# Kernel tuning notes

Hardware: AMD Instinct MI355X
Metric: run time of the kernel (lower is better)

The kernel has to match this reference:

```python
import jax, jax.numpy as jnp
import numpy as np

B, S, D = 8, 2048, 1024
N = 256          # state_dim
H = 512          # selector_hidden
E = 8            # num_experts


def murmurhash3_finalizer(token_ids):
    # Torch code works in int64 but masks to 32 bits after each multiply and
    # values stay non-negative, so it is exactly uint32 wrapping arithmetic.
    x = token_ids.astype(jnp.uint32)
    x = x ^ (x >> 16)
    x = x * jnp.uint32(2246822507)
    x = x ^ (x >> 13)
    x = x * jnp.uint32(3266489909)
    x = x ^ (x >> 16)
    return x


def setup_inputs() -> dict:
    key = jax.random.key(0)
    ks = jax.random.split(key, 7)
    scale = 0.02
    return {
        "x": jax.random.normal(ks[0], (B, S, D), dtype=jnp.float32),
        "token_ids": jax.random.randint(ks[1], (B, S), 0, 50257, dtype=jnp.int32),
        "Win": jax.random.normal(ks[2], (E, N, D), dtype=jnp.float32) * scale,      # in_proj.weight per expert
        "Wsin": jax.random.normal(ks[3], (E, H, D), dtype=jnp.float32) * scale,     # selector_in.weight
        "Wsout": jax.random.normal(ks[4], (E, 4 * N, H), dtype=jnp.float32) * scale,  # selector_out.weight
        "Wout": jax.random.normal(ks[5], (E, D, N), dtype=jnp.float32) * scale,     # out_proj.weight
        "dparam": jnp.ones((E, N), dtype=jnp.float32),                              # per-expert d
    }


def _forward(x, Win, Wsin, Wsout, Wout, dparam, token_ids):
    b, s, d = x.shape
    e_num, n, _ = Win.shape
    routes = (murmurhash3_finalizer(token_ids) % jnp.uint32(e_num)).astype(jnp.int32)  # (B,S)

    # Per-token expert projections, selected by hash route (masked accumulation
    # over the small fixed expert count; honors per-token routing).
    u = jnp.zeros((b, s, n), x.dtype)
    a = jnp.zeros((b, s, n), x.dtype)
    bg = jnp.zeros((b, s, n), x.dtype)
    c = jnp.zeros((b, s, n), x.dtype)
    dg = jnp.zeros((b, s, n), x.dtype)
    for e in range(e_num):
        m = (routes == e)[..., None]
        u = jnp.where(m, jnp.einsum('bsd,nd->bsn', x, Win[e]), u)
        sh = jax.nn.silu(jnp.einsum('bsd,hd->bsh', x, Wsin[e]))
        sel = jnp.einsum('bsh,oh->bso', sh, Wsout[e])       # (B,S,4N)
        ar, br, cr, dr = jnp.split(sel, 4, axis=-1)
        a = jnp.where(m, jax.nn.sigmoid(ar), a)
        bg = jnp.where(m, jnp.tanh(br), bg)
        c = jnp.where(m, jnp.tanh(cr), c)
        dg = jnp.where(m, jax.nn.sigmoid(dr), dg)

    dvec = dparam[routes]              # (B,S,N) expert d param per token
    skip = dvec * dg * u               # residual term, state-independent

    bidx = jnp.arange(b)

    def step(states, inp):
        # states: (B,E,N) per-expert hidden state per batch row
        route_t, u_t, a_t, b_t, c_t, skip_t = inp
        h_prev = states[bidx, route_t]                 # (B,N)
        h = a_t * h_prev + b_t * u_t
        states = states.at[bidx, route_t].set(h)       # only routed expert updates
        y = c_t * h + skip_t
        return states, y

    xs = (routes.swapaxes(0, 1), u.swapaxes(0, 1), a.swapaxes(0, 1),
          bg.swapaxes(0, 1), c.swapaxes(0, 1), skip.swapaxes(0, 1))
    states0 = jnp.zeros((b, e_num, n), x.dtype)
    _, ys = jax.lax.scan(step, states0, xs)            # ys: (S,B,N)
    y = ys.swapaxes(0, 1)                              # (B,S,N)

    out = jnp.zeros((b, s, d), x.dtype)
    for e in range(e_num):
        m = (routes == e)[..., None]
        out = jnp.where(m, jnp.einsum('bsn,dn->bsd', y, Wout[e]), out)
    return out


def reference(x, token_ids, Win, Wsin, Wsout, Wout, dparam):
    return _forward(x, Win, Wsin, Wsout, Wout, dparam, token_ids)
```

## Files before the change

### kernel.cpp

```cpp
#include <hip/hip_runtime.h>


#define TOKS 16384
#define RPAD 16512
#define DD   1024
#define NN   256
#define HH   512
#define MAXTILES  136
#define MAXCHUNKS 1088
#define CHUNK 16

typedef short short8 __attribute__((ext_vector_type(8)));
typedef float floatx4 __attribute__((ext_vector_type(4)));
typedef _Float16 half_t;

#define AS_GLOBAL __attribute__((address_space(1)))
#define AS_LDS    __attribute__((address_space(3)))

__device__ __forceinline__ void gl_lds16(const void* g, void* l) {
    __builtin_amdgcn_global_load_lds((const AS_GLOBAL void*)g, (AS_LDS void*)l, 16, 0, 0);
}

__device__ __forceinline__ unsigned short f2bf(float f) {
    union { float f; unsigned u; } c; c.f = f;
    unsigned r = c.u + 0x7FFF + ((c.u >> 16) & 1);
    return (unsigned short)(r >> 16);
}
__device__ __forceinline__ int route_of(int token) {
    unsigned x = (unsigned)token;
    x ^= x >> 16; x *= 2246822507u; x ^= x >> 13; x *= 3266489909u; x ^= x >> 16;
    return (int)(x & 7u);
}
__device__ __forceinline__ float sigm(float v) { return 1.0f / (1.0f + __expf(-v)); }
__device__ __forceinline__ float ftanh(float v) {
    float e = __expf(2.0f * v);
    return 1.0f - 2.0f / (e + 1.0f);
}

__global__ void k_route(const int* __restrict__ tok, int* __restrict__ cnt) {
    int b = blockIdx.x, tid = threadIdx.x;
    __shared__ int lc[256 * 8];
    #pragma unroll
    for (int e = 0; e < 8; e++) lc[tid * 8 + e] = 0;
    #pragma unroll
    for (int i = 0; i < 8; i++) {
        int e = route_of(tok[b * 2048 + tid * 8 + i]);
        lc[tid * 8 + e]++;
    }
    __syncthreads();
    if (tid < 8) {
        int s = 0;
        for (int t = 0; t < 256; t++) s += lc[t * 8 + tid];
        cnt[b * 8 + tid] = s;
    }
}

__global__ void k_offsets(const int* __restrict__ cnt, int* __restrict__ grpoff,
                          int* __restrict__ tileE, int* __restrict__ tileS,
                          int* __restrict__ tileR,
                          int* __restrict__ cGrp, int* __restrict__ cStart,
                          int* __restrict__ cLen, int* __restrict__ gBase,
                          int* __restrict__ meta) {
    __shared__ int sc[64], ce[8], eoff[9], etile[9], gb[65], go[64];
    int tid = threadIdx.x;
    if (tid < 64) sc[tid] = cnt[tid];
    __syncthreads();
    if (tid < 8) { int s = 0; for (int b = 0; b < 8; b++) s += sc[b * 8 + tid]; ce[tid] = s; }
    __syncthreads();
    if (tid == 0) {
        eoff[0] = 0; etile[0] = 0;
        for (int e = 0; e < 8; e++) {
            eoff[e + 1] = eoff[e] + ce[e];
            etile[e + 1] = etile[e] + (ce[e] + 127) / 128;
        }
        meta[0] = etile[8];
        gb[0] = 0;
        for (int g = 0; g < 64; g++) gb[g + 1] = gb[g] + (sc[g] + CHUNK - 1) / CHUNK;
        meta[1] = gb[64];
    }
    __syncthreads();
    if (tid < 64) {
        int b = tid >> 3, e = tid & 7;
        int run = eoff[e];
        for (int b2 = 0; b2 < b; b2++) run += sc[b2 * 8 + e];
        go[tid] = run;
        grpoff[tid] = run;
    }
    __syncthreads();
    if (tid < 8) {
        int e = tid, st = eoff[e], c = ce[e], t0 = etile[e];
        for (int i = 0, k = 0; i < c; i += 128, k++) {
            tileE[t0 + k] = e; tileS[t0 + k] = st + i;
            tileR[t0 + k] = (c - i < 128) ? (c - i) : 128;
        }
    }
    if (tid < 64) {
        int g = tid, n = sc[g], base = gb[g], s0 = go[g];
        gBase[g] = base;
        for (int i = 0, c = 0; i < n; i += CHUNK, c++) {
            cGrp[base + c] = g;
            cStart[base + c] = s0 + i;
            cLen[base + c] = (n - i < CHUNK) ? (n - i) : CHUNK;
        }
    }
}

__global__ void k_scatter(const int* __restrict__ tok, const int* __restrict__ grpoff,
                          int* __restrict__ perm) {
    int b = blockIdx.x, tid = threadIdx.x;
    __shared__ int lh[8 * 256];
    int r[8];
    int myc[8] = {0,0,0,0,0,0,0,0};
    #pragma unroll
    for (int i = 0; i < 8; i++) {
        int e = route_of(tok[b * 2048 + tid * 8 + i]);
        r[i] = e; myc[e]++;
    }
    #pragma unroll
    for (int e = 0; e < 8; e++) lh[e * 256 + tid] = myc[e];
    __syncthreads();
    for (int e = 0; e < 8; e++) {
        for (int off = 1; off < 256; off <<= 1) {
            int add = (tid >= off) ? lh[e * 256 + tid - off] : 0;
            __syncthreads();
            lh[e * 256 + tid] += add;
            __syncthreads();
        }
    }
    int basep[8];
    #pragma unroll
    for (int e = 0; e < 8; e++) basep[e] = grpoff[b * 8 + e] + lh[e * 256 + tid] - myc[e];
    #pragma unroll
    for (int i = 0; i < 8; i++) {
        int e = r[i];
        perm[basep[e]++] = b * 2048 + tid * 8 + i;
    }
}

__global__ void k_cvtw(const float* __restrict__ Win, const float* __restrict__ Wsin,
                       const float* __restrict__ Wsout, const float* __restrict__ Wout,
                       unsigned short* __restrict__ W12, unsigned short* __restrict__ Wso,
                       unsigned short* __restrict__ Wo) {
    const int C12 = 8 * 768 * 1024 / 4, CSO = 8 * 1024 * 512 / 4, CWO = 8 * 1024 * 256 / 4;
    int c = blockIdx.x * 256 + threadIdx.x;
    float4 v; unsigned short* dst;
    if (c < C12) {
        int d = c * 4;
        int e = d / (768 * 1024);
        int rem = d - e * (768 * 1024);
        int r = rem >> 10, k = rem & 1023;
        const float* src = (r < 256) ? (Win + (((size_t)e * 256 + r) << 10) + k)
                                     : (Wsin + (((size_t)e * 512 + (r - 256)) << 10) + k);
        v = *(const float4*)src;
        dst = W12 + d;
    } else if (c < C12 + CSO) {
        int d = (c - C12) * 4;
        v = *(const float4*)(Wsout + d);
        dst = Wso + d;
    } else if (c < C12 + CSO + CWO) {
        int d = (c - C12 - CSO) * 4;
        v = *(const float4*)(Wout + d);
        dst = Wo + d;
    } else return;
    ushort4 o;
    o.x = f2bf(v.x); o.y = f2bf(v.y); o.z = f2bf(v.z); o.w = f2bf(v.w);
    *(ushort4*)dst = o;
}

__global__ void k_gather(const float* __restrict__ x, const int* __restrict__ perm,
                         unsigned short* __restrict__ Xs, unsigned short* __restrict__ SHb,
                         unsigned short* __restrict__ Yb) {
    int r = blockIdx.x, t = threadIdx.x;
    if (r < TOKS) {
        int tok = perm[r];
        float4 v = *(const float4*)(x + (size_t)tok * 1024 + t * 4);
        ushort4 o;
        o.x = f2bf(v.x); o.y = f2bf(v.y); o.z = f2bf(v.z); o.w = f2bf(v.w);
        *(ushort4*)(Xs + (size_t)r * 1024 + t * 4) = o;
    } else {
        ushort4 z = {0, 0, 0, 0};
        *(ushort4*)(Xs + (size_t)r * 1024 + t * 4) = z;
        if (t < 128) *(ushort4*)(SHb + (size_t)r * 512 + t * 4) = z;
        if (t < 64)  *(ushort4*)(Yb + (size_t)r * 256 + t * 4) = z;
    }
}

template<int MODE, int KD>
__global__ __launch_bounds__(256, 4)
void k_mfma(const unsigned short* __restrict__ A, const unsigned short* __restrict__ Bw,
            const int* __restrict__ perm, const float* __restrict__ dparam,
            half_t* __restrict__ Ub, unsigned short* __restrict__ SHb,
            half_t* __restrict__ Aa, half_t* __restrict__ Wg,
            half_t* __restrict__ Cc, half_t* __restrict__ Sk,
            float* __restrict__ out,
            const int* __restrict__ tileE, const int* __restrict__ tileS,
            const int* __restrict__ tileR, const int* __restrict__ meta) {
    const int mt = blockIdx.x;
    if (mt >= meta[0]) return;
    const int e = tileE[mt], pos0 = tileS[mt], rows = tileR[mt];
    const int col0 = blockIdx.y * 64;
    const int tid = threadIdx.x;
    const int w = tid >> 6, lane = tid & 63, quad = lane >> 4, l15 = lane & 15;
    const int wm = w & 1, wn = w >> 1;
    constexpr int NOUT = (MODE == 0) ? 768 : 1024;
    constexpr int NK = KD / 32;

    __shared__ unsigned short As[3][128 * 32];
    __shared__ unsigned short Bs[3][64 * 32];

    const int r0 = tid >> 2;
    const int c8s = ((tid & 3) ^ ((tid >> 3) & 3)) * 8;
    const unsigned short* ga = A + (size_t)(pos0 + r0) * KD + c8s;
    const unsigned short* gb = Bw + ((size_t)e * NOUT + col0 + r0) * KD + c8s;

    const int sq = (quad ^ ((l15 >> 1) & 3)) * 8;
    int aoff[4], boff[2];
    #pragma unroll
    for (int i = 0; i < 4; i++) aoff[i] = (wm * 64 + i * 16 + l15) * 32 + sq;
    #pragma unroll
    for (int j = 0; j < 2; j++) boff[j] = (wn * 32 + j * 16 + l15) * 32 + sq;

    floatx4 acc[4][2] = {};

    #define STAGE(buf, k0) do { \
        gl_lds16(ga + (k0),                    As[buf] + w * 512); \
        gl_lds16(ga + (size_t)64 * KD + (k0),  As[buf] + 2048 + w * 512); \
        gl_lds16(gb + (k0),                    Bs[buf] + w * 512); \
    } while (0)

    STAGE(0, 0);
    STAGE(1, 32);
    int cur = 0, pre = 2;
    for (int kt = 0; kt < NK; kt++) {
        if (kt < NK - 1) {
            asm volatile("s_waitcnt vmcnt(3)" ::: "memory");
        } else {
            asm volatile("s_waitcnt vmcnt(0)" ::: "memory");
        }
        __builtin_amdgcn_s_barrier();
        asm volatile("" ::: "memory");
        if (kt + 2 < NK) STAGE(pre, (kt + 2) * 32);
        short8 af[4], bf[2];
        #pragma unroll
        for (int i = 0; i < 4; i++) af[i] = *(const short8*)(As[cur] + aoff[i]);
        #pragma unroll
        for (int j = 0; j < 2; j++) bf[j] = *(const short8*)(Bs[cur] + boff[j]);
        #pragma unroll
        for (int i = 0; i < 4; i++)
            #pragma unroll
            for (int j = 0; j < 2; j++)
                acc[i][j] = __builtin_amdgcn_mfma_f32_16x16x32_bf16(af[i], bf[j], acc[i][j], 0, 0, 0);
        asm volatile("s_waitcnt lgkmcnt(0)" ::: "memory");
        __builtin_amdgcn_sched_barrier(0);
        cur = (cur == 2) ? 0 : cur + 1;
        pre = (pre == 2) ? 0 : pre + 1;
    }
    #undef STAGE
    asm volatile("" ::: "memory");

    #pragma unroll
    for (int i = 0; i < 4; i++) {
        #pragma unroll
        for (int r = 0; r < 4; r++) {
            int m = wm * 64 + i * 16 + quad * 4 + r;
            if (m >= rows) continue;
            size_t row = (size_t)(pos0 + m);
            if (MODE == 0) {
                if (col0 < 256) {
                    #pragma unroll
                    for (int j = 0; j < 2; j++) {
                        int n = col0 + wn * 32 + j * 16 + l15;
                        Ub[row * 256 + n] = (half_t)acc[i][j][r];
                    }
                } else {
                    #pragma unroll
                    for (int j = 0; j < 2; j++) {
                        int n = col0 - 256 + wn * 32 + j * 16 + l15;
                        float v = acc[i][j][r];
                        SHb[row * 512 + n] = f2bf(v * sigm(v));
                    }
                }
            } else if (MODE == 1) {
                int region = col0 >> 8;
                #pragma unroll
                for (int j = 0; j < 2; j++) {
                    int n0 = (col0 & 255) + wn * 32 + j * 16 + l15;
                    size_t idx = row * 256 + (size_t)n0;
                    float v = acc[i][j][r];
                    if (region == 0) {
                        Aa[idx] = (half_t)sigm(v);
                    } else if (region == 1) {
                        Wg[idx] = (half_t)(ftanh(v) * (float)Ub[idx]);
                    } else if (region == 2) {
                        Cc[idx] = (half_t)ftanh(v);
                    } else {
                        Sk[idx] = (half_t)(dparam[e * 256 + n0] * sigm(v) * (float)Ub[idx]);
                    }
                }
            } else {
                int tok = perm[row];
                #pragma unroll
                for (int j = 0; j < 2; j++) {
                    int n = col0 + wn * 32 + j * 16 + l15;
                    out[(size_t)tok * 1024 + n] = acc[i][j][r];
                }
            }
        }
    }
}

__global__ void k_scanA(const half_t* __restrict__ Aa, const half_t* __restrict__ Wg,
                        const int* __restrict__ cStart, const int* __restrict__ cLen,
                        const int* __restrict__ meta,
                        float* __restrict__ SA, float* __restrict__ SQ) {
    int id = blockIdx.x;
    if (id >= meta[1]) return;
    int t = threadIdx.x;
    int s0 = cStart[id], L = cLen[id];
    size_t idx = (size_t)s0 * 256 + t;
    float p = 1.0f, q = 0.0f;
    for (int i = 0; i < L; i++) {
        float a = (float)Aa[idx], ww = (float)Wg[idx];
        q = a * q + ww;
        p *= a;
        idx += 256;
    }
    SA[(size_t)id * 256 + t] = p;
    SQ[(size_t)id * 256 + t] = q;
}

__global__ void k_scanB(const float* __restrict__ SA, const float* __restrict__ SQ,
                        const int* __restrict__ gBase, const int* __restrict__ cnt,
                        float* __restrict__ Hin) {
    int g = blockIdx.x, t = threadIdx.x;
    int base = gBase[g], nch = (cnt[g] + CHUNK - 1) / CHUNK;
    float h = 0.0f;
    for (int c = 0; c < nch; c++) {
        size_t k = (size_t)(base + c) * 256 + t;
        Hin[k] = h;
        h = SA[k] * h + SQ[k];
    }
}

__global__ void k_scanC(const half_t* __restrict__ Aa, const half_t* __restrict__ Wg,
                        const half_t* __restrict__ Cc, const half_t* __restrict__ Sk,
                        const int* __restrict__ cStart, const int* __restrict__ cLen,
                        const int* __restrict__ meta, const float* __restrict__ Hin,
                        unsigned short* __restrict__ Yb) {
    int id = blockIdx.x;
    if (id >= meta[1]) return;
    int t = threadIdx.x;
    int s0 = cStart[id], L = cLen[id];
    float h = Hin[(size_t)id * 256 + t];
    size_t idx = (size_t)s0 * 256 + t;
    for (int i = 0; i < L; i++) {
        float a = (float)Aa[idx], ww = (float)Wg[idx];
        float c = (float)Cc[idx], sk = (float)Sk[idx];
        h = a * h + ww;
        Yb[idx] = f2bf(c * h + sk);
        idx += 256;
    }
}

extern "C" void kernel_launch(void* const* d_in, const int* in_sizes, int n_in,
                              void* d_out, int out_size, void* d_ws, size_t ws_size,
                              hipStream_t stream) {
    const float* xin   = (const float*)d_in[0];
    const int*   tok   = (const int*)d_in[1];
    const float* Win   = (const float*)d_in[2];
    const float* Wsin  = (const float*)d_in[3];
    const float* Wsout = (const float*)d_in[4];
    const float* Wout  = (const float*)d_in[5];
    const float* dpar  = (const float*)d_in[6];
    float* out = (float*)d_out;

    size_t off = 0;
    char* base = (char*)d_ws;
    auto alloc = [&](size_t bytes) -> void* {
        void* p = base + off;
        off += (bytes + 255) & ~(size_t)255;
        return p;
    };
    half_t*         Ub  = (half_t*)alloc((size_t)RPAD * NN * 2);
    unsigned short* SHb = (unsigned short*)alloc((size_t)RPAD * HH * 2);
    unsigned short* Xs  = (unsigned short*)alloc((size_t)RPAD * DD * 2);
    unsigned short* Yb  = (unsigned short*)alloc((size_t)RPAD * NN * 2);
    half_t* Aa = (half_t*)alloc((size_t)TOKS * NN * 2);
    half_t* Wg = (half_t*)alloc((size_t)TOKS * NN * 2);
    half_t* Cc = (half_t*)alloc((size_t)TOKS * NN * 2);
    half_t* Sk = (half_t*)alloc((size_t)TOKS * NN * 2);
    unsigned short* W12 = (unsigned short*)alloc((size_t)8 * 768 * 1024 * 2);
    unsigned short* Wso = (unsigned short*)alloc((size_t)8 * 1024 * 512 * 2);
    unsigned short* Wo  = (unsigned short*)alloc((size_t)8 * 1024 * 256 * 2);
    float* SA  = (float*)alloc((size_t)MAXCHUNKS * 256 * 4);
    float* SQ  = (float*)alloc((size_t)MAXCHUNKS * 256 * 4);
    float* Hin = (float*)alloc((size_t)MAXCHUNKS * 256 * 4);
    int* perm   = (int*)alloc(TOKS * 4);
    int* cnt    = (int*)alloc(64 * 4);
    int* grpoff = (int*)alloc(64 * 4);
    int* tileE  = (int*)alloc(MAXTILES * 4);
    int* tileS  = (int*)alloc(MAXTILES * 4);
    int* tileR  = (int*)alloc(MAXTILES * 4);
    int* cGrp   = (int*)alloc(MAXCHUNKS * 4);
    int* cStart = (int*)alloc(MAXCHUNKS * 4);
    int* cLen   = (int*)alloc(MAXCHUNKS * 4);
    int* gBase  = (int*)alloc(64 * 4);
    int* meta   = (int*)alloc(16 * 4);

    k_route<<<8, 256, 0, stream>>>(tok, cnt);
    k_offsets<<<1, 256, 0, stream>>>(cnt, grpoff, tileE, tileS, tileR,
                                     cGrp, cStart, cLen, gBase, meta);
    k_scatter<<<8, 256, 0, stream>>>(tok, grpoff, perm);
    k_cvtw<<<12288, 256, 0, stream>>>(Win, Wsin, Wsout, Wout, W12, Wso, Wo);
    k_gather<<<RPAD, 256, 0, stream>>>(xin, perm, Xs, SHb, Yb);

    k_mfma<0, 1024><<<dim3(MAXTILES, 12), 256, 0, stream>>>(Xs, W12, perm, dpar,
        Ub, SHb, Aa, Wg, Cc, Sk, out, tileE, tileS, tileR, meta);
    k_mfma<1, 512><<<dim3(MAXTILES, 16), 256, 0, stream>>>(SHb, Wso, perm, dpar,
        Ub, SHb, Aa, Wg, Cc, Sk, out, tileE, tileS, tileR, meta);

    k_scanA<<<MAXCHUNKS, 256, 0, stream>>>(Aa, Wg, cStart, cLen, meta, SA, SQ);
    k_scanB<<<64, 256, 0, stream>>>(SA, SQ, gBase, cnt, Hin);
    k_scanC<<<MAXCHUNKS, 256, 0, stream>>>(Aa, Wg, Cc, Sk, cStart, cLen, meta, Hin, Yb);

    k_mfma<2, 256><<<dim3(MAXTILES, 16), 256, 0, stream>>>(Yb, Wo, perm, dpar,
        Ub, SHb, Aa, Wg, Cc, Sk, out, tileE, tileS, tileR, meta);
}
```

Before: 341.4 us.

## Interleave scan gate arrays, fuse convert/gather kernels, warp-shuffle scatter scan, MFMA priority

```diff
diff --git a/kernel.cpp b/kernel.cpp
--- a/kernel.cpp
+++ b/kernel.cpp
@@ -9,6 +9,7 @@
 #define MAXTILES  136
 #define MAXCHUNKS 1088
 #define CHUNK 16
+#define CVTBLKS 12288
 
 typedef short short8 __attribute__((ext_vector_type(8)));
 typedef float floatx4 __attribute__((ext_vector_type(4)));
@@ -36,6 +37,8 @@
     float e = __expf(2.0f * v);
     return 1.0f - 2.0f / (e + 1.0f);
 }
+
+union H2 { unsigned u; half_t h[2]; };
 
 __global__ void k_route(const int* __restrict__ tok, int* __restrict__ cnt) {
     int b = blockIdx.x, tid = threadIdx.x;
@@ -108,7 +111,8 @@
 __global__ void k_scatter(const int* __restrict__ tok, const int* __restrict__ grpoff,
                           int* __restrict__ perm) {
     int b = blockIdx.x, tid = threadIdx.x;
-    __shared__ int lh[8 * 256];
+    int lane = tid & 63, w = tid >> 6;
+    __shared__ unsigned wsum[4][4];
     int r[8];
     int myc[8] = {0,0,0,0,0,0,0,0};
     #pragma unroll
@@ -116,20 +120,35 @@
         int e = route_of(tok[b * 2048 + tid * 8 + i]);
         r[i] = e; myc[e]++;
     }
-    #pragma unroll
-    for (int e = 0; e < 8; e++) lh[e * 256 + tid] = myc[e];
-    __syncthreads();
+    unsigned p[4], v[4];
+    #pragma unroll
+    for (int k = 0; k < 4; k++) {
+        p[k] = (unsigned)myc[2 * k] | ((unsigned)myc[2 * k + 1] << 16);
+        v[k] = p[k];
+    }
+    #pragma unroll
+    for (int off = 1; off < 64; off <<= 1) {
+        #pragma unroll
+        for (int k = 0; k < 4; k++) {
+            unsigned o = __shfl_up(v[k], off, 64);
+            if (lane >= off) v[k] += o;
+        }
+    }
+    if (lane == 63) {
+        #pragma unroll
+        for (int k = 0; k < 4; k++) wsum[w][k] = v[k];
+    }
+    __syncthreads();
+    unsigned add[4] = {0, 0, 0, 0};
+    for (int ww = 0; ww < w; ww++)
+        #pragma unroll
+        for (int k = 0; k < 4; k++) add[k] += wsum[ww][k];
+    int basep[8];
+    #pragma unroll
     for (int e = 0; e < 8; e++) {
-        for (int off = 1; off < 256; off <<= 1) {
-            int add = (tid >= off) ? lh[e * 256 + tid - off] : 0;
-            __syncthreads();
-            lh[e * 256 + tid] += add;
-            __syncthreads();
-        }
-    }
-    int basep[8];
-    #pragma unroll
-    for (int e = 0; e < 8; e++) basep[e] = grpoff[b * 8 + e] + lh[e * 256 + tid] - myc[e];
+        unsigned ex = v[e >> 1] + add[e >> 1] - p[e >> 1];
+        basep[e] = grpoff[b * 8 + e] + (int)((e & 1) ? (ex >> 16) : (ex & 0xffffu));
+    }
     #pragma unroll
     for (int i = 0; i < 8; i++) {
         int e = r[i];
@@ -137,51 +156,53 @@
     }
 }
 
-__global__ void k_cvtw(const float* __restrict__ Win, const float* __restrict__ Wsin,
+__global__ void k_prep(const float* __restrict__ Win, const float* __restrict__ Wsin,
                        const float* __restrict__ Wsout, const float* __restrict__ Wout,
                        unsigned short* __restrict__ W12, unsigned short* __restrict__ Wso,
-                       unsigned short* __restrict__ Wo) {
-    const int C12 = 8 * 768 * 1024 / 4, CSO = 8 * 1024 * 512 / 4, CWO = 8 * 1024 * 256 / 4;
-    int c = blockIdx.x * 256 + threadIdx.x;
-    float4 v; unsigned short* dst;
-    if (c < C12) {
-        int d = c * 4;
-        int e = d / (768 * 1024);
-        int rem = d - e * (768 * 1024);
-        int r = rem >> 10, k = rem & 1023;
-        const float* src = (r < 256) ? (Win + (((size_t)e * 256 + r) << 10) + k)
-                                     : (Wsin + (((size_t)e * 512 + (r - 256)) << 10) + k);
-        v = *(const float4*)src;
-        dst = W12 + d;
-    } else if (c < C12 + CSO) {
-        int d = (c - C12) * 4;
-        v = *(const float4*)(Wsout + d);
-        dst = Wso + d;
-    } else if (c < C12 + CSO + CWO) {
-        int d = (c - C12 - CSO) * 4;
-        v = *(const float4*)(Wout + d);
-        dst = Wo + d;
-    } else return;
-    ushort4 o;
-    o.x = f2bf(v.x); o.y = f2bf(v.y); o.z = f2bf(v.z); o.w = f2bf(v.w);
-    *(ushort4*)dst = o;
-}
-
-__global__ void k_gather(const float* __restrict__ x, const int* __restrict__ perm,
-                         unsigned short* __restrict__ Xs, unsigned short* __restrict__ SHb,
-                         unsigned short* __restrict__ Yb) {
-    int r = blockIdx.x, t = threadIdx.x;
-    if (r < TOKS) {
-        int tok = perm[r];
-        float4 v = *(const float4*)(x + (size_t)tok * 1024 + t * 4);
+                       unsigned short* __restrict__ Wo,
+                       const float* __restrict__ x, const int* __restrict__ perm,
+                       unsigned short* __restrict__ Xs, unsigned short* __restrict__ SHb,
+                       unsigned short* __restrict__ Yb) {
+    int blk = blockIdx.x, tid = threadIdx.x;
+    if (blk < CVTBLKS) {
+        const int C12 = 8 * 768 * 1024 / 4, CSO = 8 * 1024 * 512 / 4, CWO = 8 * 1024 * 256 / 4;
+        int c = blk * 256 + tid;
+        float4 v; unsigned short* dst;
+        if (c < C12) {
+            int d = c * 4;
+            int e = d / (768 * 1024);
+            int rem = d - e * (768 * 1024);
+            int r = rem >> 10, k = rem & 1023;
+            const float* src = (r < 256) ? (Win + (((size_t)e * 256 + r) << 10) + k)
+                                         : (Wsin + (((size_t)e * 512 + (r - 256)) << 10) + k);
+            v = *(const float4*)src;
+            dst = W12 + d;
+        } else if (c < C12 + CSO) {
+            int d = (c - C12) * 4;
+            v = *(const float4*)(Wsout + d);
+            dst = Wso + d;
+        } else {
+            int d = (c - C12 - CSO) * 4;
+            v = *(const float4*)(Wout + d);
+            dst = Wo + d;
+        }
         ushort4 o;
         o.x = f2bf(v.x); o.y = f2bf(v.y); o.z = f2bf(v.z); o.w = f2bf(v.w);
-        *(ushort4*)(Xs + (size_t)r * 1024 + t * 4) = o;
+        *(ushort4*)dst = o;
     } else {
-        ushort4 z = {0, 0, 0, 0};
-        *(ushort4*)(Xs + (size_t)r * 1024 + t * 4) = z;
-        if (t < 128) *(ushort4*)(SHb + (size_t)r * 512 + t * 4) = z;
-        if (t < 64)  *(ushort4*)(Yb + (size_t)r * 256 + t * 4) = z;
+        int r = blk - CVTBLKS;
+        if (r < TOKS) {
+            int tok = perm[r];
+            float4 v = *(const float4*)(x + (size_t)tok * 1024 + tid * 4);
+            ushort4 o;
+            o.x = f2bf(v.x); o.y = f2bf(v.y); o.z = f2bf(v.z); o.w = f2bf(v.w);
+            *(ushort4*)(Xs + (size_t)r * 1024 + tid * 4) = o;
+        } else {
+            ushort4 z = {0, 0, 0, 0};
+            *(ushort4*)(Xs + (size_t)r * 1024 + tid * 4) = z;
+            if (tid < 128) *(ushort4*)(SHb + (size_t)r * 512 + tid * 4) = z;
+            if (tid < 64)  *(ushort4*)(Yb + (size_t)r * 256 + tid * 4) = z;
+        }
     }
 }
 
@@ -190,8 +211,7 @@
 void k_mfma(const unsigned short* __restrict__ A, const unsigned short* __restrict__ Bw,
             const int* __restrict__ perm, const float* __restrict__ dparam,
             half_t* __restrict__ Ub, unsigned short* __restrict__ SHb,
-            half_t* __restrict__ Aa, half_t* __restrict__ Wg,
-            half_t* __restrict__ Cc, half_t* __restrict__ Sk,
+            half_t* __restrict__ AW, half_t* __restrict__ CS,
             float* __restrict__ out,
             const int* __restrict__ tileE, const int* __restrict__ tileS,
             const int* __restrict__ tileR, const int* __restrict__ meta) {
@@ -245,11 +265,13 @@
         for (int i = 0; i < 4; i++) af[i] = *(const short8*)(As[cur] + aoff[i]);
         #pragma unroll
         for (int j = 0; j < 2; j++) bf[j] = *(const short8*)(Bs[cur] + boff[j]);
+        __builtin_amdgcn_s_setprio(1);
         #pragma unroll
         for (int i = 0; i < 4; i++)
             #pragma unroll
             for (int j = 0; j < 2; j++)
                 acc[i][j] = __builtin_amdgcn_mfma_f32_16x16x32_bf16(af[i], bf[j], acc[i][j], 0, 0, 0);
+        __builtin_amdgcn_s_setprio(0);
         asm volatile("s_waitcnt lgkmcnt(0)" ::: "memory");
         __builtin_amdgcn_sched_barrier(0);
         cur = (cur == 2) ? 0 : cur + 1;
@@ -285,16 +307,16 @@
                 #pragma unroll
                 for (int j = 0; j < 2; j++) {
                     int n0 = (col0 & 255) + wn * 32 + j * 16 + l15;
-                    size_t idx = row * 256 + (size_t)n0;
                     float v = acc[i][j][r];
+                    size_t rb = row * 512 + (size_t)n0 * 2;
                     if (region == 0) {
-                        Aa[idx] = (half_t)sigm(v);
+                        AW[rb] = (half_t)sigm(v);
                     } else if (region == 1) {
-                        Wg[idx] = (half_t)(ftanh(v) * (float)Ub[idx]);
+                        AW[rb + 1] = (half_t)(ftanh(v) * (float)Ub[row * 256 + n0]);
                     } else if (region == 2) {
-                        Cc[idx] = (half_t)ftanh(v);
+                        CS[rb] = (half_t)ftanh(v);
                     } else {
-                        Sk[idx] = (half_t)(dparam[e * 256 + n0] * sigm(v) * (float)Ub[idx]);
+                        CS[rb + 1] = (half_t)(dparam[e * 256 + n0] * sigm(v) * (float)Ub[row * 256 + n0]);
                     }
                 }
             } else {
@@ -309,7 +331,7 @@
     }
 }
 
-__global__ void k_scanA(const half_t* __restrict__ Aa, const half_t* __restrict__ Wg,
+__global__ void k_scanA(const half_t* __restrict__ AW,
                         const int* __restrict__ cStart, const int* __restrict__ cLen,
                         const int* __restrict__ meta,
                         float* __restrict__ SA, float* __restrict__ SQ) {
@@ -317,10 +339,12 @@
     if (id >= meta[1]) return;
     int t = threadIdx.x;
     int s0 = cStart[id], L = cLen[id];
+    const unsigned* AW32 = (const unsigned*)AW;
     size_t idx = (size_t)s0 * 256 + t;
     float p = 1.0f, q = 0.0f;
     for (int i = 0; i < L; i++) {
-        float a = (float)Aa[idx], ww = (float)Wg[idx];
+        H2 cv; cv.u = AW32[idx];
+        float a = (float)cv.h[0], ww = (float)cv.h[1];
         q = a * q + ww;
         p *= a;
         idx += 256;
@@ -342,8 +366,7 @@
     }
 }
 
-__global__ void k_scanC(const half_t* __restrict__ Aa, const half_t* __restrict__ Wg,
-                        const half_t* __restrict__ Cc, const half_t* __restrict__ Sk,
+__global__ void k_scanC(const half_t* __restrict__ AW, const half_t* __restrict__ CS,
                         const int* __restrict__ cStart, const int* __restrict__ cLen,
                         const int* __restrict__ meta, const float* __restrict__ Hin,
                         unsigned short* __restrict__ Yb) {
@@ -351,11 +374,15 @@
     if (id >= meta[1]) return;
     int t = threadIdx.x;
     int s0 = cStart[id], L = cLen[id];
+    const unsigned* AW32 = (const unsigned*)AW;
+    const unsigned* CS32 = (const unsigned*)CS;
     float h = Hin[(size_t)id * 256 + t];
     size_t idx = (size_t)s0 * 256 + t;
     for (int i = 0; i < L; i++) {
-        float a = (float)Aa[idx], ww = (float)Wg[idx];
-        float c = (float)Cc[idx], sk = (float)Sk[idx];
+        H2 av; av.u = AW32[idx];
+        H2 cv; cv.u = CS32[idx];
+        float a = (float)av.h[0], ww = (float)av.h[1];
+        float c = (float)cv.h[0], sk = (float)cv.h[1];
         h = a * h + ww;
         Yb[idx] = f2bf(c * h + sk);
         idx += 256;
@@ -385,10 +412,8 @@
     unsigned short* SHb = (unsigned short*)alloc((size_t)RPAD * HH * 2);
     unsigned short* Xs  = (unsigned short*)alloc((size_t)RPAD * DD * 2);
     unsigned short* Yb  = (unsigned short*)alloc((size_t)RPAD * NN * 2);
-    half_t* Aa = (half_t*)alloc((size_t)TOKS * NN * 2);
-    half_t* Wg = (half_t*)alloc((size_t)TOKS * NN * 2);
-    half_t* Cc = (half_t*)alloc((size_t)TOKS * NN * 2);
-    half_t* Sk = (half_t*)alloc((size_t)TOKS * NN * 2);
+    half_t* AW = (half_t*)alloc((size_t)TOKS * NN * 4);
+    half_t* CS = (half_t*)alloc((size_t)TOKS * NN * 4);
     unsigned short* W12 = (unsigned short*)alloc((size_t)8 * 768 * 1024 * 2);
     unsigned short* Wso = (unsigned short*)alloc((size_t)8 * 1024 * 512 * 2);
     unsigned short* Wo  = (unsigned short*)alloc((size_t)8 * 1024 * 256 * 2);
@@ -411,18 +436,18 @@
     k_offsets<<<1, 256, 0, stream>>>(cnt, grpoff, tileE, tileS, tileR,
                                      cGrp, cStart, cLen, gBase, meta);
     k_scatter<<<8, 256, 0, stream>>>(tok, grpoff, perm);
-    k_cvtw<<<12288, 256, 0, stream>>>(Win, Wsin, Wsout, Wout, W12, Wso, Wo);
-    k_gather<<<RPAD, 256, 0, stream>>>(xin, perm, Xs, SHb, Yb);
+    k_prep<<<CVTBLKS + RPAD, 256, 0, stream>>>(Win, Wsin, Wsout, Wout, W12, Wso, Wo,
+                                               xin, perm, Xs, SHb, Yb);
 
     k_mfma<0, 1024><<<dim3(MAXTILES, 12), 256, 0, stream>>>(Xs, W12, perm, dpar,
-        Ub, SHb, Aa, Wg, Cc, Sk, out, tileE, tileS, tileR, meta);
+        Ub, SHb, AW, CS, out, tileE, tileS, tileR, meta);
     k_mfma<1, 512><<<dim3(MAXTILES, 16), 256, 0, stream>>>(SHb, Wso, perm, dpar,
-        Ub, SHb, Aa, Wg, Cc, Sk, out, tileE, tileS, tileR, meta);
-
-    k_scanA<<<MAXCHUNKS, 256, 0, stream>>>(Aa, Wg, cStart, cLen, meta, SA, SQ);
+        Ub, SHb, AW, CS, out, tileE, tileS, tileR, meta);
+
+    k_scanA<<<MAXCHUNKS, 256, 0, stream>>>(AW, cStart, cLen, meta, SA, SQ);
     k_scanB<<<64, 256, 0, stream>>>(SA, SQ, gBase, cnt, Hin);
-    k_scanC<<<MAXCHUNKS, 256, 0, stream>>>(Aa, Wg, Cc, Sk, cStart, cLen, meta, Hin, Yb);
+    k_scanC<<<MAXCHUNKS, 256, 0, stream>>>(AW, CS, cStart, cLen, meta, Hin, Yb);
 
     k_mfma<2, 256><<<dim3(MAXTILES, 16), 256, 0, stream>>>(Yb, Wo, perm, dpar,
-        Ub, SHb, Aa, Wg, Cc, Sk, out, tileE, tileS, tileR, meta);
-}
+        Ub, SHb, AW, CS, out, tileE, tileS, tileR, meta);
+}
```

Result: no change. 336.5 us (-1.4%).
